# Kernel tuning notes

Hardware: AMD Instinct MI355X
Metric: run time of the kernel (lower is better)

## Reference

```python
import jax, jax.numpy as jnp
import numpy as np

B, N, C = 8, 2048, 256

def setup_inputs() -> dict:
    key = jax.random.key(0)
    ks = jax.random.split(key, 6)
    corr = jax.random.normal(ks[0], (B, N, N), dtype=jnp.float32)
    feat = jax.random.normal(ks[1], (B, N, C), dtype=jnp.float32)
    histogram = jax.random.uniform(ks[2], (B, N, 1), dtype=jnp.float32)
    mask = jax.random.normal(ks[3], (N, N), dtype=jnp.float32)
    # nn.Linear(C, C) params
    lim = 1.0 / np.sqrt(C)
    v_w = jax.random.uniform(ks[4], (C, C), minval=-lim, maxval=lim, dtype=jnp.float32)
    v_b = jax.random.uniform(ks[5], (C,), minval=-lim, maxval=lim, dtype=jnp.float32)
    return {"corr": corr, "feat": feat, "histogram": histogram, "mask": mask, "v_w": v_w, "v_b": v_b}

def reference(corr, feat, histogram, mask, v_w, v_b):
    # histogram is viewed/expanded in the original but never used downstream.
    # masked softmax over last axis: (b, n, n)
    attn = jax.nn.softmax(corr + mask[None, :, :], axis=-1)
    # v projection: y = feat @ v_w.T + v_b   (b, n, c)
    ref_feat_v = jnp.einsum("bnc,dc->bnd", feat, v_w) + v_b
    # attention output: (b, n, c)
    return jnp.einsum("bnm,bmc->bnc", attn, ref_feat_v)
```

## Files before the change

kernel.cpp:

```cpp
#include <hip/hip_runtime.h>
#include <hip/hip_fp16.h>


#define B_ 8
#define N_ 2048
#define C_ 256

typedef _Float16 half8  __attribute__((ext_vector_type(8)));
typedef _Float16 half4v __attribute__((ext_vector_type(4)));
typedef float    f32x4  __attribute__((ext_vector_type(4)));

static __device__ __forceinline__ void gload16(const void* g, void* l) {
    __builtin_amdgcn_global_load_lds(
        (const __attribute__((address_space(1))) unsigned int*)g,
        (__attribute__((address_space(3))) unsigned int*)l, 16, 0, 0);
}

__global__ __launch_bounds__(256) void k_convw(const float* __restrict__ w,
                                               _Float16* __restrict__ wh) {
    int i = (blockIdx.x * 256 + threadIdx.x) * 4;
    float4 v = *(const float4*)(w + i);
    half4v h = {(_Float16)v.x, (_Float16)v.y, (_Float16)v.z, (_Float16)v.w};
    *(half4v*)(wh + i) = h;
}

__global__ __launch_bounds__(256) void k_trans(const float* __restrict__ feat,
                                               _Float16* __restrict__ featF) {
    __shared__ _Float16 s[64][68];
    int blk  = blockIdx.x;
    int b    = blk >> 7;
    int tile = blk & 127;
    int n0   = (tile >> 2) << 6;
    int c0   = (tile & 3) << 6;
    int t    = threadIdx.x;

    const float* src = feat + ((size_t)(b * N_ + n0)) * C_ + c0;
#pragma unroll
    for (int i = 0; i < 4; ++i) {
        int idx = i * 256 + t;
        int row = idx >> 4;
        int c4  = (idx & 15) << 2;
        float4 v = *(const float4*)(src + (size_t)row * C_ + c4);
        half4v h = {(_Float16)v.x, (_Float16)v.y, (_Float16)v.z, (_Float16)v.w};
        *(half4v*)&s[row][c4] = h;
    }
    __syncthreads();

    int w = t >> 6, l = t & 63;
    int kk  = w & 1;
    int cb0 = (w >> 1) << 1;
#pragma unroll
    for (int cbi = 0; cbi < 2; ++cbi) {
        int cb = cb0 + cbi;
        half8 v;
#pragma unroll
        for (int j = 0; j < 8; ++j)
            v[j] = s[kk * 32 + ((l >> 4) << 3) + j][(cb << 4) + (l & 15)];
        _Float16* dst = featF +
            (((size_t)((b * 64 + (n0 >> 5) + kk) * 16 + (c0 >> 4) + cb)) * 64 + l) * 8;
        *(half8*)dst = v;
    }
}

__global__ __launch_bounds__(256) void k_expm(const float* __restrict__ mask,
                                              _Float16* __restrict__ expmF) {
    __shared__ float s[64][68];
    int nb4 = blockIdx.x >> 5;
    int kb2 = blockIdx.x & 31;
    int t   = threadIdx.x;

    const float* src = mask + ((size_t)(nb4 * 64)) * N_ + kb2 * 64;
#pragma unroll
    for (int i = 0; i < 4; ++i) {
        int idx = i * 256 + t;
        int row = idx >> 4;
        int c4  = (idx & 15) << 2;
        float4 v = *(const float4*)(src + (size_t)row * N_ + c4);
        s[row][c4 + 0] = __expf(v.x);
        s[row][c4 + 1] = __expf(v.y);
        s[row][c4 + 2] = __expf(v.z);
        s[row][c4 + 3] = __expf(v.w);
    }
    __syncthreads();

    int w = t >> 6, l = t & 63;
#pragma unroll
    for (int kbl = 0; kbl < 2; ++kbl) {
        half8 v;
#pragma unroll
        for (int j = 0; j < 8; ++j)
            v[j] = (_Float16)s[w * 16 + (l & 15)][kbl * 32 + ((l >> 4) << 3) + j];
        _Float16* dst = expmF +
            (((size_t)(nb4 * 4 + w)) * 64 + kb2 * 2 + kbl) * 512 + l * 8;
        *(half8*)dst = v;
    }
}

__global__ __launch_bounds__(512, 2) void k_attn(const float* __restrict__ corr,
                                                 const _Float16* __restrict__ expmF,
                                                 const _Float16* __restrict__ featF,
                                                 _Float16* __restrict__ T) {
    __shared__ float    c_lds[2][64 * 128];
    __shared__ _Float16 f_lds[64 * 512];

    const int blk = blockIdx.x;
    const int b   = blk & 7;
    const int sg  = blk >> 3;
    const int r0  = sg * 64;
    const int tg  = threadIdx.x;
    const int w   = tg >> 6, l = tg & 63;
    const int wr  = w >> 1, wc = w & 1;
    const int lrow = l & 15, kch = l >> 4;

    const float*    pcorr = corr + ((size_t)(b * N_ + r0)) * N_;
    const _Float16* pex   = expmF + ((size_t)(sg * 4 + wr)) * 64 * 512 + l * 8;
    const _Float16* pfb   = featF + (size_t)b * 524288;

    f32x4 acc[8] = {};
    float rs = 0.0f;

#define STAGE_CORR(SS)                                                        \
    { _Pragma("unroll")                                                       \
      for (int i_ = 0; i_ < 4; ++i_) {                                        \
        int rpair = w * 8 + i_ * 2;                                           \
        int row   = rpair + (l >> 5);                                         \
        int ch    = l & 31;                                                   \
        int grp   = (ch >> 1) ^ (row & 15);                                   \
        gload16(pcorr + (size_t)row * N_ + (SS) * 128 + grp * 8 + (ch & 1) * 4, \
                &c_lds[(SS) & 1][rpair * 128]);                               \
      } }

#define STAGE_F(SS)                                                           \
    { _Pragma("unroll")                                                       \
      for (int i_ = 0; i_ < 8; ++i_) {                                        \
        int cid = w * 8 + i_;                                                 \
        gload16(pfb + (((size_t)(SS) * 4 + (cid >> 4)) * 16 + (cid & 15)) * 512 + l * 8, \
                &f_lds[cid * 512]);                                           \
      } }

#define SUBSTEP(SSB, SUB, EK0, EK1)                                           \
    {                                                                         \
        const float* cl = &c_lds[SSB][(wr * 16 + lrow) * 128];                \
        int s0 = ((SUB) * 8 + kch) ^ lrow;                                    \
        int s1 = ((SUB) * 8 + 4 + kch) ^ lrow;                                \
        f32x4 c00 = *(const f32x4*)(cl + s0 * 8);                             \
        f32x4 c01 = *(const f32x4*)(cl + s0 * 8 + 4);                         \
        f32x4 c10 = *(const f32x4*)(cl + s1 * 8);                             \
        f32x4 c11 = *(const f32x4*)(cl + s1 * 8 + 4);                         \
        half8 a0, a1;                                                         \
        _Pragma("unroll")                                                     \
        for (int j = 0; j < 4; ++j) {                                         \
            float p0 = __expf(c00[j]) * (float)EK0[j];                        \
            rs += p0; a0[j] = (_Float16)p0;                                   \
            float p1 = __expf(c01[j]) * (float)EK0[4 + j];                    \
            rs += p1; a0[4 + j] = (_Float16)p1;                               \
            float p2 = __expf(c10[j]) * (float)EK1[j];                        \
            rs += p2; a1[j] = (_Float16)p2;                                   \
            float p3 = __expf(c11[j]) * (float)EK1[4 + j];                    \
            rs += p3; a1[4 + j] = (_Float16)p3;                               \
        }                                                                     \
        _Pragma("unroll")                                                     \
        for (int n = 0; n < 8; ++n) {                                         \
            half8 b0 = *(const half8*)&f_lds[(((SUB) * 2 + 0) * 16 + wc * 8 + n) * 512 + l * 8]; \
            half8 b1 = *(const half8*)&f_lds[(((SUB) * 2 + 1) * 16 + wc * 8 + n) * 512 + l * 8]; \
            acc[n] = __builtin_amdgcn_mfma_f32_16x16x32_f16(a0, b0, acc[n], 0, 0, 0); \
            acc[n] = __builtin_amdgcn_mfma_f32_16x16x32_f16(a1, b1, acc[n], 0, 0, 0); \
        }                                                                     \
    }

#define SSBODY(SS, EC0, EC1, EC2, EC3, EN0, EN1, EN2, EN3)                    \
    {                                                                         \
        if ((SS) < 15) { asm volatile("s_waitcnt vmcnt(8)" ::: "memory"); }   \
        else           { asm volatile("s_waitcnt vmcnt(0)" ::: "memory"); }   \
        __builtin_amdgcn_sched_barrier(0);                                    \
        __builtin_amdgcn_s_barrier();                                         \
        __builtin_amdgcn_sched_barrier(0);                                    \
        SUBSTEP((SS) & 1, 0, EC0, EC1);                                       \
        SUBSTEP((SS) & 1, 1, EC2, EC3);                                       \
        asm volatile("s_waitcnt lgkmcnt(0)" ::: "memory");                    \
        __builtin_amdgcn_sched_barrier(0);                                    \
        __builtin_amdgcn_s_barrier();                                         \
        __builtin_amdgcn_sched_barrier(0);                                    \
        if ((SS) < 15) {                                                      \
            STAGE_F((SS) + 1);                                                \
            __builtin_amdgcn_sched_barrier(0);                                \
            EN0 = *(const half8*)(pex + (size_t)(4 * (SS) + 4) * 512);        \
            EN1 = *(const half8*)(pex + (size_t)(4 * (SS) + 5) * 512);        \
            EN2 = *(const half8*)(pex + (size_t)(4 * (SS) + 6) * 512);        \
            EN3 = *(const half8*)(pex + (size_t)(4 * (SS) + 7) * 512);        \
            __builtin_amdgcn_sched_barrier(0);                                \
            if ((SS) < 14) STAGE_CORR((SS) + 2);                              \
            __builtin_amdgcn_sched_barrier(0);                                \
        }                                                                     \
    }

    half8 eA0, eA1, eA2, eA3, eB0, eB1, eB2, eB3;
    STAGE_CORR(0);
    __builtin_amdgcn_sched_barrier(0);
    STAGE_F(0);
    __builtin_amdgcn_sched_barrier(0);
    eA0 = *(const half8*)(pex + (size_t)0 * 512);
    eA1 = *(const half8*)(pex + (size_t)1 * 512);
    eA2 = *(const half8*)(pex + (size_t)2 * 512);
    eA3 = *(const half8*)(pex + (size_t)3 * 512);
    __builtin_amdgcn_sched_barrier(0);
    STAGE_CORR(1);
    __builtin_amdgcn_sched_barrier(0);

    for (int sh = 0; sh < 8; ++sh) {
        SSBODY(2 * sh,     eA0, eA1, eA2, eA3, eB0, eB1, eB2, eB3);
        SSBODY(2 * sh + 1, eB0, eB1, eB2, eB3, eA0, eA1, eA2, eA3);
    }
#undef SSBODY
#undef SUBSTEP
#undef STAGE_F
#undef STAGE_CORR

    rs += __shfl_xor(rs, 16);
    rs += __shfl_xor(rs, 32);
    float inv = 1.0f / rs;

    _Float16* pT = T + ((size_t)(b * N_ + r0 + wr * 16 + kch * 4)) * C_
                     + wc * 128 + lrow;
#pragma unroll
    for (int j = 0; j < 4; ++j) {
        float invj = __shfl(inv, kch * 4 + j);
#pragma unroll
        for (int n = 0; n < 8; ++n) {
            pT[(size_t)j * C_ + n * 16] = (_Float16)(acc[n][j] * invj);
        }
    }
}

__global__ __launch_bounds__(256, 2) void k_out(const _Float16* __restrict__ T,
                                                const _Float16* __restrict__ wh,
                                                const float* __restrict__ v_b,
                                                float* __restrict__ out) {
    const int blk = blockIdx.x;
    const int r0  = blk * 32;
    const int t   = threadIdx.x;
    const int w   = t >> 6, l = t & 63;
    const int wr  = w >> 1, wc = w & 1;
    const int lrow = l & 15, kch = l >> 4;

    const _Float16* pA = T  + ((size_t)(r0 + wr * 16 + lrow)) * C_ + kch * 8;
    const _Float16* pB = wh + ((size_t)(wc * 128 + lrow)) * C_ + kch * 8;

    f32x4 acc[8] = {};
#pragma unroll
    for (int step = 0; step < 8; step++) {
        half8 a = *(const half8*)(pA + step * 32);
#pragma unroll
        for (int q = 0; q < 8; q++) {
            half8 bf = *(const half8*)(pB + step * 32 + (size_t)q * 16 * C_);
            acc[q] = __builtin_amdgcn_mfma_f32_16x16x32_f16(a, bf, acc[q], 0, 0, 0);
        }
    }

    float* pO = out + ((size_t)(r0 + wr * 16 + kch * 4)) * C_ + wc * 128 + lrow;
#pragma unroll
    for (int q = 0; q < 8; q++) {
        float bias = v_b[wc * 128 + q * 16 + lrow];
#pragma unroll
        for (int j = 0; j < 4; j++) {
            pO[(size_t)j * C_ + q * 16] = acc[q][j] + bias;
        }
    }
}

extern "C" void kernel_launch(void* const* d_in, const int* in_sizes, int n_in,
                              void* d_out, int out_size, void* d_ws, size_t ws_size,
                              hipStream_t stream) {
    const float* corr = (const float*)d_in[0];
    const float* feat = (const float*)d_in[1];
    const float* mask = (const float*)d_in[3];
    const float* v_w  = (const float*)d_in[4];
    const float* v_b  = (const float*)d_in[5];
    float* out = (float*)d_out;

    char* ws = (char*)d_ws;
    _Float16* featF = (_Float16*)ws;
    _Float16* T     = (_Float16*)(ws + (size_t)8 * 1024 * 1024);
    _Float16* wh    = (_Float16*)(ws + (size_t)16 * 1024 * 1024);
    _Float16* expmF = (_Float16*)(ws + (size_t)17 * 1024 * 1024);

    hipLaunchKernelGGL(k_trans, dim3(1024), dim3(256), 0, stream, feat, featF);
    hipLaunchKernelGGL(k_expm,  dim3(1024), dim3(256), 0, stream, mask, expmF);
    hipLaunchKernelGGL(k_convw, dim3(64),   dim3(256), 0, stream, v_w, wh);
    hipLaunchKernelGGL(k_attn,  dim3(256),  dim3(512), 0, stream, corr, expmF, featF, T);
    hipLaunchKernelGGL(k_out,   dim3(512),  dim3(256), 0, stream, T, wh, v_b, out);
}
```

Before: 87.11 us.

## Apply value projection before attention and fuse bias into attention epilogue

Reorders the computation so feat is projected by v_w first (new k_gemm that converts feat to fp16, runs MFMA, and writes the result in the fragment layout k_attn expects). Attention then consumes the projected values and writes fp32 output with the bias added after normalization, which removes the fp16 intermediate T and the separate k_out GEMM launch. Because softmax rows sum to one, adding the bias after normalization is equivalent. The projected values are now rounded to fp16 before the attention matmul, which changes numerical error slightly.

After: 76.53 us. -12.1%, faster.

```diff
diff --git a/kernel.cpp b/kernel.cpp
--- a/kernel.cpp
+++ b/kernel.cpp
@@ -16,49 +16,80 @@
         (__attribute__((address_space(3))) unsigned int*)l, 16, 0, 0);
 }
 
-__global__ __launch_bounds__(256) void k_convw(const float* __restrict__ w,
-                                               _Float16* __restrict__ wh) {
-    int i = (blockIdx.x * 256 + threadIdx.x) * 4;
-    float4 v = *(const float4*)(w + i);
-    half4v h = {(_Float16)v.x, (_Float16)v.y, (_Float16)v.z, (_Float16)v.w};
-    *(half4v*)(wh + i) = h;
-}
-
-__global__ __launch_bounds__(256) void k_trans(const float* __restrict__ feat,
-                                               _Float16* __restrict__ featF) {
-    __shared__ _Float16 s[64][68];
-    int blk  = blockIdx.x;
-    int b    = blk >> 7;
-    int tile = blk & 127;
-    int n0   = (tile >> 2) << 6;
-    int c0   = (tile & 3) << 6;
-    int t    = threadIdx.x;
-
-    const float* src = feat + ((size_t)(b * N_ + n0)) * C_ + c0;
-#pragma unroll
-    for (int i = 0; i < 4; ++i) {
-        int idx = i * 256 + t;
-        int row = idx >> 4;
-        int c4  = (idx & 15) << 2;
-        float4 v = *(const float4*)(src + (size_t)row * C_ + c4);
-        half4v h = {(_Float16)v.x, (_Float16)v.y, (_Float16)v.z, (_Float16)v.w};
-        *(half4v*)&s[row][c4] = h;
-    }
+__global__ __launch_bounds__(64) void k_whf(const float* __restrict__ w,
+                                            _Float16* __restrict__ whF) {
+    int f  = blockIdx.x;
+    int cb = f >> 4, db = f & 15;
+    int l  = threadIdx.x;
+    const float* src = w + (size_t)(db * 16 + (l & 15)) * C_ + cb * 32 + (l >> 4) * 8;
+    half8 v;
+#pragma unroll
+    for (int j = 0; j < 8; ++j) v[j] = (_Float16)src[j];
+    *(half8*)(whF + (size_t)f * 512 + l * 8) = v;
+}
+
+__global__ __launch_bounds__(512, 2) void k_gemm(const float* __restrict__ feat,
+                                                 const _Float16* __restrict__ whF,
+                                                 _Float16* __restrict__ featG) {
+    __shared__ float s_feat[64 * 256];
+
+    const int blk = blockIdx.x;
+    const int b   = blk & 7;
+    const int rg  = blk >> 3;
+    const int r0  = rg * 64;
+    const int tg  = threadIdx.x;
+    const int w   = tg >> 6, l = tg & 63;
+    const int wr  = w >> 1, wc = w & 1;
+    const int lrow = l & 15, kch = l >> 4;
+
+    const float* pf = feat + ((size_t)(b * N_ + r0)) * C_;
+#pragma unroll
+    for (int i = 0; i < 8; ++i) {
+        int c   = i * 512 + tg;
+        int row = c >> 6;
+        int ch  = c & 63;
+        int grp = (ch >> 1) ^ (row & 15);
+        gload16(pf + (size_t)row * C_ + grp * 8 + (ch & 1) * 4,
+                (char*)s_feat + (size_t)c * 16);
+    }
+    asm volatile("s_waitcnt vmcnt(0)" ::: "memory");
+    __builtin_amdgcn_s_barrier();
+
+    f32x4 acc[8] = {};
+#pragma unroll
+    for (int cb = 0; cb < 8; ++cb) {
+        const float* cl = &s_feat[(wr * 16 + lrow) * 256];
+        int slot = (cb * 4 + kch) ^ lrow;
+        f32x4 c0 = *(const f32x4*)(cl + slot * 8);
+        f32x4 c1 = *(const f32x4*)(cl + slot * 8 + 4);
+        half8 a;
+#pragma unroll
+        for (int j = 0; j < 4; ++j) { a[j] = (_Float16)c0[j]; a[4 + j] = (_Float16)c1[j]; }
+#pragma unroll
+        for (int n = 0; n < 8; ++n) {
+            half8 bf = *(const half8*)(whF + (size_t)((cb * 16 + wc * 8 + n) * 512) + l * 8);
+            acc[n] = __builtin_amdgcn_mfma_f32_16x16x32_f16(a, bf, acc[n], 0, 0, 0);
+        }
+    }
+
     __syncthreads();
-
-    int w = t >> 6, l = t & 63;
-    int kk  = w & 1;
-    int cb0 = (w >> 1) << 1;
-#pragma unroll
-    for (int cbi = 0; cbi < 2; ++cbi) {
-        int cb = cb0 + cbi;
+    _Float16* t = (_Float16*)s_feat;
+#pragma unroll
+    for (int n = 0; n < 8; ++n)
+#pragma unroll
+        for (int j = 0; j < 4; ++j)
+            t[(size_t)(wr * 16 + kch * 4 + j) * 264 + wc * 128 + n * 16 + lrow] =
+                (_Float16)acc[n][j];
+    __syncthreads();
+#pragma unroll
+    for (int q = 0; q < 4; ++q) {
+        int f  = w * 4 + q;
+        int nb = f >> 4, db = f & 15;
         half8 v;
 #pragma unroll
         for (int j = 0; j < 8; ++j)
-            v[j] = s[kk * 32 + ((l >> 4) << 3) + j][(cb << 4) + (l & 15)];
-        _Float16* dst = featF +
-            (((size_t)((b * 64 + (n0 >> 5) + kk) * 16 + (c0 >> 4) + cb)) * 64 + l) * 8;
-        *(half8*)dst = v;
+            v[j] = t[(size_t)(nb * 32 + kch * 8 + j) * 264 + db * 16 + lrow];
+        *(half8*)(featG + ((size_t)((b * 64 + rg * 2 + nb) * 16 + db)) * 512 + l * 8) = v;
     }
 }
 
@@ -98,8 +129,9 @@
 
 __global__ __launch_bounds__(512, 2) void k_attn(const float* __restrict__ corr,
                                                  const _Float16* __restrict__ expmF,
-                                                 const _Float16* __restrict__ featF,
-                                                 _Float16* __restrict__ T) {
+                                                 const _Float16* __restrict__ featG,
+                                                 const float* __restrict__ vb,
+                                                 float* __restrict__ out) {
     __shared__ float    c_lds[2][64 * 128];
     __shared__ _Float16 f_lds[64 * 512];
 
@@ -114,7 +146,7 @@
 
     const float*    pcorr = corr + ((size_t)(b * N_ + r0)) * N_;
     const _Float16* pex   = expmF + ((size_t)(sg * 4 + wr)) * 64 * 512 + l * 8;
-    const _Float16* pfb   = featF + (size_t)b * 524288;
+    const _Float16* pfb   = featG + (size_t)b * 524288;
 
     f32x4 acc[8] = {};
     float rs = 0.0f;
@@ -220,50 +252,18 @@
     rs += __shfl_xor(rs, 32);
     float inv = 1.0f / rs;
 
-    _Float16* pT = T + ((size_t)(b * N_ + r0 + wr * 16 + kch * 4)) * C_
-                     + wc * 128 + lrow;
+    float bias[8];
+#pragma unroll
+    for (int n = 0; n < 8; ++n) bias[n] = vb[wc * 128 + n * 16 + lrow];
+
+    float* pO = out + ((size_t)(b * N_ + r0 + wr * 16 + kch * 4)) * C_
+                    + wc * 128 + lrow;
 #pragma unroll
     for (int j = 0; j < 4; ++j) {
         float invj = __shfl(inv, kch * 4 + j);
 #pragma unroll
         for (int n = 0; n < 8; ++n) {
-            pT[(size_t)j * C_ + n * 16] = (_Float16)(acc[n][j] * invj);
-        }
-    }
-}
-
-__global__ __launch_bounds__(256, 2) void k_out(const _Float16* __restrict__ T,
-                                                const _Float16* __restrict__ wh,
-                                                const float* __restrict__ v_b,
-                                                float* __restrict__ out) {
-    const int blk = blockIdx.x;
-    const int r0  = blk * 32;
-    const int t   = threadIdx.x;
-    const int w   = t >> 6, l = t & 63;
-    const int wr  = w >> 1, wc = w & 1;
-    const int lrow = l & 15, kch = l >> 4;
-
-    const _Float16* pA = T  + ((size_t)(r0 + wr * 16 + lrow)) * C_ + kch * 8;
-    const _Float16* pB = wh + ((size_t)(wc * 128 + lrow)) * C_ + kch * 8;
-
-    f32x4 acc[8] = {};
-#pragma unroll
-    for (int step = 0; step < 8; step++) {
-        half8 a = *(const half8*)(pA + step * 32);
-#pragma unroll
-        for (int q = 0; q < 8; q++) {
-            half8 bf = *(const half8*)(pB + step * 32 + (size_t)q * 16 * C_);
-            acc[q] = __builtin_amdgcn_mfma_f32_16x16x32_f16(a, bf, acc[q], 0, 0, 0);
-        }
-    }
-
-    float* pO = out + ((size_t)(r0 + wr * 16 + kch * 4)) * C_ + wc * 128 + lrow;
-#pragma unroll
-    for (int q = 0; q < 8; q++) {
-        float bias = v_b[wc * 128 + q * 16 + lrow];
-#pragma unroll
-        for (int j = 0; j < 4; j++) {
-            pO[(size_t)j * C_ + q * 16] = acc[q][j] + bias;
+            pO[(size_t)j * C_ + n * 16] = acc[n][j] * invj + bias[n];
         }
     }
 }
@@ -279,14 +279,12 @@
     float* out = (float*)d_out;
 
     char* ws = (char*)d_ws;
-    _Float16* featF = (_Float16*)ws;
-    _Float16* T     = (_Float16*)(ws + (size_t)8 * 1024 * 1024);
-    _Float16* wh    = (_Float16*)(ws + (size_t)16 * 1024 * 1024);
-    _Float16* expmF = (_Float16*)(ws + (size_t)17 * 1024 * 1024);
-
-    hipLaunchKernelGGL(k_trans, dim3(1024), dim3(256), 0, stream, feat, featF);
-    hipLaunchKernelGGL(k_expm,  dim3(1024), dim3(256), 0, stream, mask, expmF);
-    hipLaunchKernelGGL(k_convw, dim3(64),   dim3(256), 0, stream, v_w, wh);
-    hipLaunchKernelGGL(k_attn,  dim3(256),  dim3(512), 0, stream, corr, expmF, featF, T);
-    hipLaunchKernelGGL(k_out,   dim3(512),  dim3(256), 0, stream, T, wh, v_b, out);
-}
+    _Float16* featG = (_Float16*)ws;
+    _Float16* expmF = (_Float16*)(ws + (size_t)8 * 1024 * 1024);
+    _Float16* whF   = (_Float16*)(ws + (size_t)16 * 1024 * 1024);
+
+    hipLaunchKernelGGL(k_whf,  dim3(128),  dim3(64),  0, stream, v_w, whF);
+    hipLaunchKernelGGL(k_gemm, dim3(256),  dim3(512), 0, stream, feat, whF, featG);
+    hipLaunchKernelGGL(k_expm, dim3(1024), dim3(256), 0, stream, mask, expmF);
+    hipLaunchKernelGGL(k_attn, dim3(256),  dim3(512), 0, stream, corr, expmF, featG, v_b, out);
+}
```
